# Kernel optimization log

Measured on AMD Instinct MI355X. Metric: run time of the kernel, lower is better.

The kernel has to match this reference:

```python
import jax, jax.numpy as jnp
import numpy as np

LAMBD = 1.0
N_CLASSES = 1000


def setup_inputs() -> dict:
    key = jax.random.key(0)
    k1, k2, k3 = jax.random.split(key, 3)
    B, D, C = 32768, 128, N_CLASSES
    embeddings = jax.random.normal(k1, (B, D), dtype=jnp.float32)
    targets = jax.random.randint(k2, (B,), 0, C, dtype=jnp.int64)
    centers = jax.random.normal(k3, (C, D), dtype=jnp.float32)
    return {"embeddings": embeddings, "targets": targets, "centers": centers}


def reference(embeddings, targets, centers):
    # Original code round-trips embeddings through numpy -> data_mat is detached.
    e = jax.lax.stop_gradient(embeddings)  # [B, D]
    B = e.shape[0]
    C = centers.shape[0]
    # intra-class distance: exact per-sample gather + squared diff
    own_centers = centers[targets]                         # [B, D]
    dis_intra = jnp.sum((e - own_centers) ** 2, axis=1)    # [B]
    # all-pairs squared distances via expansion (avoids [B, C, D] intermediate)
    e_sq = jnp.sum(e * e, axis=1)                          # [B]
    c_sq = jnp.sum(centers * centers, axis=1)              # [C]
    cross = jnp.einsum('bd,cd->bc', e, centers)            # [B, C]
    dis_all = e_sq[:, None] + c_sq[None, :] - 2.0 * cross  # [B, C]
    # margin terms over non-target classes only
    mask = targets[:, None] != jnp.arange(C)[None, :]      # [B, C] True where j != y_i
    terms = jax.nn.relu(LAMBD + dis_intra[:, None] - dis_all)
    loss = jnp.sum(jnp.where(mask, terms, 0.0)) / (B * (C - 1))
    return loss
```

## Files before the change

kernel.cpp:

```cpp
#include <hip/hip_runtime.h>

#define DD 128

typedef __attribute__((ext_vector_type(8))) short short8;
typedef __attribute__((ext_vector_type(4))) float f32x4;

typedef __attribute__((address_space(1))) const void gvoid_t;
typedef __attribute__((address_space(3))) void svoid_t;
#define GLOAD_LDS16(g, s) __builtin_amdgcn_global_load_lds((gvoid_t*)(g), (svoid_t*)(s), 16, 0, 0)

__device__ __forceinline__ unsigned int f2bf(float f) {
    unsigned int x = __builtin_bit_cast(unsigned int, f);
    return (x + 0x7fffu + ((x >> 16) & 1u)) >> 16;
}
__device__ __forceinline__ unsigned int pack2(float a, float b) {
    return f2bf(a) | (f2bf(b) << 16);
}

__global__ void prep_centers(const float* __restrict__ ctr,
                             unsigned char* __restrict__ wsB,
                             float* __restrict__ csqh, int C, int Cpad) {
    int gid = blockIdx.x * 256 + threadIdx.x;
    int col = gid >> 2, q = gid & 3;
    if (col >= Cpad) return;
    const float* src = ctr + (size_t)col * DD + q * 32;
    float cs = 0.f;
    #pragma unroll
    for (int j = 0; j < 4; ++j) {
        float4 v0 = make_float4(0.f,0.f,0.f,0.f), v1 = v0;
        if (col < C) {
            v0 = *(const float4*)(src + j * 8);
            v1 = *(const float4*)(src + j * 8 + 4);
        }
        cs = fmaf(v0.x,v0.x,cs); cs = fmaf(v0.y,v0.y,cs);
        cs = fmaf(v0.z,v0.z,cs); cs = fmaf(v0.w,v0.w,cs);
        cs = fmaf(v1.x,v1.x,cs); cs = fmaf(v1.y,v1.y,cs);
        cs = fmaf(v1.z,v1.z,cs); cs = fmaf(v1.w,v1.w,cs);
        uint4 w;
        w.x = pack2(v0.x, v0.y); w.y = pack2(v0.z, v0.w);
        w.z = pack2(v1.x, v1.y); w.w = pack2(v1.z, v1.w);
        int r = col & 127;
        unsigned off = (unsigned)(col >> 7) * 32768u + (unsigned)r * 256u +
                       ((((unsigned)q * 4u + j) * 16u) ^ (((unsigned)r & 7u) << 4));
        *(uint4*)(wsB + off) = w;
    }
    cs += __shfl_xor(cs, 1);
    cs += __shfl_xor(cs, 2);
    if (q == 0) csqh[col] = (col < C) ? 0.5f * cs : 1e30f;
}

__global__ __launch_bounds__(256, 2) void center_mfma(
    const float* __restrict__ emb, const int* __restrict__ tgt,
    const float* __restrict__ ctr, const unsigned char* __restrict__ wsB,
    const float* __restrict__ csqh, float* __restrict__ partials,
    int B, int C, int NT)
{
    __shared__ uint4 sA4[1024];
    __shared__ uint4 sB4[2048];
    __shared__ float sRT[64];
    __shared__ float sRed[4];
    unsigned char* sAb = (unsigned char*)sA4;
    unsigned char* sBb = (unsigned char*)sB4;

    const int t = threadIdx.x;
    const int row0 = blockIdx.x * 64;

    {
        const int r = t >> 2, q = t & 3;
        const float* srcE = emb + (size_t)(row0 + r) * DD + q * 32;
        const int y = tgt[row0 + r];
        const float* srcC = ctr + (size_t)y * DD + q * 32;
        float se = 0.f, sd = 0.f;
        #pragma unroll
        for (int j = 0; j < 4; ++j) {
            float4 e0 = *(const float4*)(srcE + j * 8);
            float4 e1 = *(const float4*)(srcE + j * 8 + 4);
            float4 c0 = *(const float4*)(srcC + j * 8);
            float4 c1 = *(const float4*)(srcC + j * 8 + 4);
            se = fmaf(e0.x,e0.x,se); se = fmaf(e0.y,e0.y,se);
            se = fmaf(e0.z,e0.z,se); se = fmaf(e0.w,e0.w,se);
            se = fmaf(e1.x,e1.x,se); se = fmaf(e1.y,e1.y,se);
            se = fmaf(e1.z,e1.z,se); se = fmaf(e1.w,e1.w,se);
            float d;
            d = e0.x-c0.x; sd = fmaf(d,d,sd);  d = e0.y-c0.y; sd = fmaf(d,d,sd);
            d = e0.z-c0.z; sd = fmaf(d,d,sd);  d = e0.w-c0.w; sd = fmaf(d,d,sd);
            d = e1.x-c1.x; sd = fmaf(d,d,sd);  d = e1.y-c1.y; sd = fmaf(d,d,sd);
            d = e1.z-c1.z; sd = fmaf(d,d,sd);  d = e1.w-c1.w; sd = fmaf(d,d,sd);
            uint4 w;
            w.x = pack2(e0.x, e0.y); w.y = pack2(e0.z, e0.w);
            w.z = pack2(e1.x, e1.y); w.w = pack2(e1.z, e1.w);
            unsigned off = (unsigned)r * 256u +
                ((((unsigned)q * 4u + j) * 16u) ^ (((unsigned)r & 7u) << 4));
            *(uint4*)(sAb + off) = w;
        }
        se += __shfl_xor(se, 1); se += __shfl_xor(se, 2);
        sd += __shfl_xor(sd, 1); sd += __shfl_xor(sd, 2);
        if (q == 0) sRT[r] = 0.5f * (1.0f + sd - se);
    }
    __syncthreads();

    const int l  = t & 63;
    const int w  = t >> 6;
    const int li = l & 15;
    const int lh = l >> 4;
    const unsigned swz = ((unsigned)li & 7u) << 4;

    short8 aF[4][4];
    #pragma unroll
    for (int mf = 0; mf < 4; ++mf)
        #pragma unroll
        for (int ks = 0; ks < 4; ++ks)
            aF[mf][ks] = *(const short8*)(sAb + (unsigned)(li + 16*mf) * 256u +
                                          (((unsigned)(16*lh + 64*ks)) ^ swz));
    float rtv[16];
    #pragma unroll
    for (int mf = 0; mf < 4; ++mf)
        #pragma unroll
        for (int rr = 0; rr < 4; ++rr)
            rtv[mf*4+rr] = sRT[16*mf + 4*lh + rr];

    float tsum = 0.f;

    for (int nt = 0; nt < NT; ++nt) {
        __syncthreads();
        const unsigned char* g = wsB + (size_t)nt * 32768;
        #pragma unroll
        for (int i = 0; i < 8; ++i) {
            unsigned off = (unsigned)(i * 256 + t) * 16u;
            GLOAD_LDS16(g + off, sBb + off);
        }
        float cq0 = csqh[nt*128 + w*32 + li];
        float cq1 = csqh[nt*128 + w*32 + 16 + li];
        __syncthreads();

        f32x4 acc[4][2];
        #pragma unroll
        for (int mf = 0; mf < 4; ++mf)
            #pragma unroll
            for (int rr = 0; rr < 4; ++rr) {
                acc[mf][0][rr] = rtv[mf*4+rr] - cq0;
                acc[mf][1][rr] = rtv[mf*4+rr] - cq1;
            }

        #pragma unroll
        for (int ks = 0; ks < 4; ++ks) {
            unsigned kof = ((unsigned)(16*lh + 64*ks)) ^ swz;
            short8 b0 = *(const short8*)(sBb + (unsigned)(li + 32*w) * 256u + kof);
            short8 b1 = *(const short8*)(sBb + (unsigned)(li + 16 + 32*w) * 256u + kof);
            #pragma unroll
            for (int mf = 0; mf < 4; ++mf) {
                acc[mf][0] = __builtin_amdgcn_mfma_f32_16x16x32_bf16(aF[mf][ks], b0, acc[mf][0], 0, 0, 0);
                acc[mf][1] = __builtin_amdgcn_mfma_f32_16x16x32_bf16(aF[mf][ks], b1, acc[mf][1], 0, 0, 0);
            }
        }

        float s0 = 0.f, s1 = 0.f;
        #pragma unroll
        for (int mf = 0; mf < 4; ++mf)
            #pragma unroll
            for (int rr = 0; rr < 4; ++rr) {
                s0 = fmaf(2.0f, fmaxf(acc[mf][0][rr], 0.f), s0);
                s1 = fmaf(2.0f, fmaxf(acc[mf][1][rr], 0.f), s1);
            }
        tsum += s0 + s1;
    }

    float s = tsum;
    #pragma unroll
    for (int off = 32; off; off >>= 1) s += __shfl_down(s, off);
    if (l == 0) sRed[w] = s;
    __syncthreads();
    if (t == 0) partials[blockIdx.x] = sRed[0] + sRed[1] + sRed[2] + sRed[3];
}

__global__ void reduce_k(const float* __restrict__ partials, int n,
                         float* __restrict__ out, double diagSub, double invDenom) {
    __shared__ double sRed[4];
    int t = threadIdx.x;
    double s = 0.0;
    for (int i = t; i < n; i += 256) s += (double)partials[i];
    #pragma unroll
    for (int off = 32; off; off >>= 1) s += __shfl_down(s, off);
    if ((t & 63) == 0) sRed[t >> 6] = s;
    __syncthreads();
    if (t == 0) out[0] = (float)(((sRed[0]+sRed[1]+sRed[2]+sRed[3]) - diagSub) * invDenom);
}

extern "C" void kernel_launch(void* const* d_in, const int* in_sizes, int n_in,
                              void* d_out, int out_size, void* d_ws, size_t ws_size,
                              hipStream_t stream) {
    const float* emb = (const float*)d_in[0];
    const int*   tgt = (const int*)d_in[1];
    const float* ctr = (const float*)d_in[2];

    const int B = in_sizes[1];
    const int C = in_sizes[2] / DD;
    const int NT = (C + 127) / 128;
    const int Cpad = NT * 128;
    const int nblk = B / 64;

    unsigned char* wsB = (unsigned char*)d_ws;
    float* csqh     = (float*)(wsB + (size_t)NT * 32768);
    float* partials = csqh + Cpad;

    prep_centers<<<(Cpad * 4 + 255) / 256, 256, 0, stream>>>(ctr, wsB, csqh, C, Cpad);
    center_mfma<<<nblk, 256, 0, stream>>>(emb, tgt, ctr, wsB, csqh, partials, B, C, NT);
    reduce_k<<<1, 256, 0, stream>>>(partials, nblk, (float*)d_out,
                                    (double)B * 1.0,
                                    1.0 / ((double)B * (double)(C - 1)));
}
```

Measured before the change: 27.38 us.

## Prefetch next center tile during MFMA, fuse final reduction via atomics

The main loop now reads B fragments into registers, then issues the global-to-LDS load for the next center tile before running the MFMAs, so the load overlaps compute. The separate reduce kernel is replaced by a fixed-point 64-bit atomic accumulation with a last-block-done counter, and a memset resets the counter. prep_centers runs twice as many threads with half the work each, and bf16 packing switches to the HIP intrinsic. Risks: fixed-point quantization of per-block sums and an extra memset launch.

Result: slower. 36.74 us (+34.2%).

```diff
diff --git a/kernel.cpp b/kernel.cpp
--- a/kernel.cpp
+++ b/kernel.cpp
@@ -1,4 +1,5 @@
 #include <hip/hip_runtime.h>
+#include <hip/hip_bf16.h>
 
 #define DD 128
 
@@ -9,24 +10,27 @@
 typedef __attribute__((address_space(3))) void svoid_t;
 #define GLOAD_LDS16(g, s) __builtin_amdgcn_global_load_lds((gvoid_t*)(g), (svoid_t*)(s), 16, 0, 0)
 
-__device__ __forceinline__ unsigned int f2bf(float f) {
-    unsigned int x = __builtin_bit_cast(unsigned int, f);
-    return (x + 0x7fffu + ((x >> 16) & 1u)) >> 16;
-}
-__device__ __forceinline__ unsigned int pack2(float a, float b) {
-    return f2bf(a) | (f2bf(b) << 16);
+__device__ __forceinline__ unsigned pack2(float a, float b) {
+    __hip_bfloat162 h = __float22bfloat162_rn(make_float2(a, b));
+    unsigned u;
+    __builtin_memcpy(&u, &h, 4);
+    return u;
 }
 
 __global__ void prep_centers(const float* __restrict__ ctr,
                              unsigned char* __restrict__ wsB,
                              float* __restrict__ csqh, int C, int Cpad) {
     int gid = blockIdx.x * 256 + threadIdx.x;
-    int col = gid >> 2, q = gid & 3;
+    int col = gid >> 3, q = (gid >> 1) & 3, jh = gid & 1;
     if (col >= Cpad) return;
     const float* src = ctr + (size_t)col * DD + q * 32;
+    const int r = col & 127;
+    const unsigned base = (unsigned)(col >> 7) * 32768u + (unsigned)r * 256u;
+    const unsigned sw = ((unsigned)r & 7u) << 4;
     float cs = 0.f;
     #pragma unroll
-    for (int j = 0; j < 4; ++j) {
+    for (int jj = 0; jj < 2; ++jj) {
+        int j = jh * 2 + jj;
         float4 v0 = make_float4(0.f,0.f,0.f,0.f), v1 = v0;
         if (col < C) {
             v0 = *(const float4*)(src + j * 8);
@@ -39,21 +43,17 @@
         uint4 w;
         w.x = pack2(v0.x, v0.y); w.y = pack2(v0.z, v0.w);
         w.z = pack2(v1.x, v1.y); w.w = pack2(v1.z, v1.w);
-        int r = col & 127;
-        unsigned off = (unsigned)(col >> 7) * 32768u + (unsigned)r * 256u +
-                       ((((unsigned)q * 4u + j) * 16u) ^ (((unsigned)r & 7u) << 4));
-        *(uint4*)(wsB + off) = w;
-    }
-    cs += __shfl_xor(cs, 1);
-    cs += __shfl_xor(cs, 2);
-    if (q == 0) csqh[col] = (col < C) ? 0.5f * cs : 1e30f;
+        *(uint4*)(wsB + base + ((((unsigned)q * 4u + j) * 16u) ^ sw)) = w;
+    }
+    cs += __shfl_xor(cs, 1); cs += __shfl_xor(cs, 2); cs += __shfl_xor(cs, 4);
+    if ((gid & 7) == 0) csqh[col] = (col < C) ? 0.5f * cs : 1e30f;
 }
 
 __global__ __launch_bounds__(256, 2) void center_mfma(
     const float* __restrict__ emb, const int* __restrict__ tgt,
     const float* __restrict__ ctr, const unsigned char* __restrict__ wsB,
-    const float* __restrict__ csqh, float* __restrict__ partials,
-    int B, int C, int NT)
+    const float* __restrict__ csqh, unsigned long long* __restrict__ ctl,
+    float* __restrict__ out, int C, int NT, double diagSub, double invDenom)
 {
     __shared__ uint4 sA4[1024];
     __shared__ uint4 sB4[2048];
@@ -86,12 +86,12 @@
             d = e0.z-c0.z; sd = fmaf(d,d,sd);  d = e0.w-c0.w; sd = fmaf(d,d,sd);
             d = e1.x-c1.x; sd = fmaf(d,d,sd);  d = e1.y-c1.y; sd = fmaf(d,d,sd);
             d = e1.z-c1.z; sd = fmaf(d,d,sd);  d = e1.w-c1.w; sd = fmaf(d,d,sd);
-            uint4 w;
-            w.x = pack2(e0.x, e0.y); w.y = pack2(e0.z, e0.w);
-            w.z = pack2(e1.x, e1.y); w.w = pack2(e1.z, e1.w);
+            uint4 wv;
+            wv.x = pack2(e0.x, e0.y); wv.y = pack2(e0.z, e0.w);
+            wv.z = pack2(e1.x, e1.y); wv.w = pack2(e1.z, e1.w);
             unsigned off = (unsigned)r * 256u +
                 ((((unsigned)q * 4u + j) * 16u) ^ (((unsigned)r & 7u) << 4));
-            *(uint4*)(sAb + off) = w;
+            *(uint4*)(sAb + off) = wv;
         }
         se += __shfl_xor(se, 1); se += __shfl_xor(se, 2);
         sd += __shfl_xor(sd, 1); sd += __shfl_xor(sd, 2);
@@ -119,19 +119,40 @@
         for (int rr = 0; rr < 4; ++rr)
             rtv[mf*4+rr] = sRT[16*mf + 4*lh + rr];
 
+    #pragma unroll
+    for (int i = 0; i < 8; ++i) {
+        unsigned off = (unsigned)(i * 256 + t) * 16u;
+        GLOAD_LDS16(wsB + off, sBb + off);
+    }
+    float cqA = csqh[w*32 + li];
+    float cqB = csqh[w*32 + 16 + li];
+
     float tsum = 0.f;
 
     for (int nt = 0; nt < NT; ++nt) {
         __syncthreads();
-        const unsigned char* g = wsB + (size_t)nt * 32768;
-        #pragma unroll
-        for (int i = 0; i < 8; ++i) {
-            unsigned off = (unsigned)(i * 256 + t) * 16u;
-            GLOAD_LDS16(g + off, sBb + off);
-        }
-        float cq0 = csqh[nt*128 + w*32 + li];
-        float cq1 = csqh[nt*128 + w*32 + 16 + li];
+
+        const float cq0 = cqA, cq1 = cqB;
+
+        short8 bF0[4], bF1[4];
+        #pragma unroll
+        for (int ks = 0; ks < 4; ++ks) {
+            unsigned kof = ((unsigned)(16*lh + 64*ks)) ^ swz;
+            bF0[ks] = *(const short8*)(sBb + (unsigned)(li + 32*w) * 256u + kof);
+            bF1[ks] = *(const short8*)(sBb + (unsigned)(li + 16 + 32*w) * 256u + kof);
+        }
         __syncthreads();
+
+        if (nt + 1 < NT) {
+            const unsigned char* g = wsB + (size_t)(nt + 1) * 32768;
+            #pragma unroll
+            for (int i = 0; i < 8; ++i) {
+                unsigned off = (unsigned)(i * 256 + t) * 16u;
+                GLOAD_LDS16(g + off, sBb + off);
+            }
+            cqA = csqh[(nt+1)*128 + w*32 + li];
+            cqB = csqh[(nt+1)*128 + w*32 + 16 + li];
+        }
 
         f32x4 acc[4][2];
         #pragma unroll
@@ -143,16 +164,12 @@
             }
 
         #pragma unroll
-        for (int ks = 0; ks < 4; ++ks) {
-            unsigned kof = ((unsigned)(16*lh + 64*ks)) ^ swz;
-            short8 b0 = *(const short8*)(sBb + (unsigned)(li + 32*w) * 256u + kof);
-            short8 b1 = *(const short8*)(sBb + (unsigned)(li + 16 + 32*w) * 256u + kof);
+        for (int ks = 0; ks < 4; ++ks)
             #pragma unroll
             for (int mf = 0; mf < 4; ++mf) {
-                acc[mf][0] = __builtin_amdgcn_mfma_f32_16x16x32_bf16(aF[mf][ks], b0, acc[mf][0], 0, 0, 0);
-                acc[mf][1] = __builtin_amdgcn_mfma_f32_16x16x32_bf16(aF[mf][ks], b1, acc[mf][1], 0, 0, 0);
-            }
-        }
+                acc[mf][0] = __builtin_amdgcn_mfma_f32_16x16x32_bf16(aF[mf][ks], bF0[ks], acc[mf][0], 0, 0, 0);
+                acc[mf][1] = __builtin_amdgcn_mfma_f32_16x16x32_bf16(aF[mf][ks], bF1[ks], acc[mf][1], 0, 0, 0);
+            }
 
         float s0 = 0.f, s1 = 0.f;
         #pragma unroll
@@ -170,20 +187,17 @@
     for (int off = 32; off; off >>= 1) s += __shfl_down(s, off);
     if (l == 0) sRed[w] = s;
     __syncthreads();
-    if (t == 0) partials[blockIdx.x] = sRed[0] + sRed[1] + sRed[2] + sRed[3];
-}
-
-__global__ void reduce_k(const float* __restrict__ partials, int n,
-                         float* __restrict__ out, double diagSub, double invDenom) {
-    __shared__ double sRed[4];
-    int t = threadIdx.x;
-    double s = 0.0;
-    for (int i = t; i < n; i += 256) s += (double)partials[i];
-    #pragma unroll
-    for (int off = 32; off; off >>= 1) s += __shfl_down(s, off);
-    if ((t & 63) == 0) sRed[t >> 6] = s;
-    __syncthreads();
-    if (t == 0) out[0] = (float)(((sRed[0]+sRed[1]+sRed[2]+sRed[3]) - diagSub) * invDenom);
+    if (t == 0) {
+        float bs = sRed[0] + sRed[1] + sRed[2] + sRed[3];
+        unsigned long long q = (unsigned long long)((double)bs * 4096.0 + 0.5);
+        atomicAdd(&ctl[0], q);
+        __threadfence();
+        unsigned old = atomicAdd((unsigned*)&ctl[1], 1u);
+        if (old == (unsigned)gridDim.x - 1u) {
+            unsigned long long tot = atomicAdd(&ctl[0], 0ULL);
+            out[0] = (float)(((double)tot * (1.0 / 4096.0) - diagSub) * invDenom);
+        }
+    }
 }
 
 extern "C" void kernel_launch(void* const* d_in, const int* in_sizes, int n_in,
@@ -200,12 +214,13 @@
     const int nblk = B / 64;
 
     unsigned char* wsB = (unsigned char*)d_ws;
-    float* csqh     = (float*)(wsB + (size_t)NT * 32768);
-    float* partials = csqh + Cpad;
-
-    prep_centers<<<(Cpad * 4 + 255) / 256, 256, 0, stream>>>(ctr, wsB, csqh, C, Cpad);
-    center_mfma<<<nblk, 256, 0, stream>>>(emb, tgt, ctr, wsB, csqh, partials, B, C, NT);
-    reduce_k<<<1, 256, 0, stream>>>(partials, nblk, (float*)d_out,
-                                    (double)B * 1.0,
-                                    1.0 / ((double)B * (double)(C - 1)));
-}
+    float* csqh = (float*)(wsB + (size_t)NT * 32768);
+    unsigned long long* ctl = (unsigned long long*)(csqh + Cpad);
+
+    (void)hipMemsetAsync(ctl, 0, 16, stream);
+    prep_centers<<<(Cpad * 8) / 256, 256, 0, stream>>>(ctr, wsB, csqh, C, Cpad);
+    center_mfma<<<nblk, 256, 0, stream>>>(emb, tgt, ctr, wsB, csqh, ctl,
+                                          (float*)d_out, C, NT,
+                                          (double)B,
+                                          1.0 / ((double)B * (double)(C - 1)));
+}
```
